# Kernel optimization log

Measured on AMD Instinct MI355X. Metric: run time of the kernel, lower is better.

## Reference

```python
import jax, jax.numpy as jnp
import numpy as np

B, T, D, H = 2048, 512, 32, 64


def _gru_layer(x, W_ih, W_hh, b_ih, b_hh):
    # x: [B, T, Din]; W_ih: [3H, Din]; W_hh: [3H, H]; gate order r, z, n (PyTorch).
    xp = jnp.einsum('btd,gd->btg', x, W_ih) + b_ih  # precompute input projections [B,T,3H]

    def step(h, xt):
        gh = h @ W_hh.T + b_hh                      # [B,3H]
        ir, iz, inn = jnp.split(xt, 3, axis=-1)
        hr, hz, hn = jnp.split(gh, 3, axis=-1)
        r = jax.nn.sigmoid(ir + hr)
        z = jax.nn.sigmoid(iz + hz)
        n = jnp.tanh(inn + r * hn)
        h_new = (1.0 - z) * n + z * h
        return h_new, h_new

    h0 = jnp.zeros((x.shape[0], W_hh.shape[1]), dtype=x.dtype)
    _, ys = jax.lax.scan(step, h0, xp.transpose(1, 0, 2))  # ys: [T,B,H]
    return ys.transpose(1, 0, 2)                           # [B,T,H]


def setup_inputs() -> dict:
    key = jax.random.key(0)
    ks = jax.random.split(key, 12)
    s_in = 1.0 / np.sqrt(H)
    u = lambda k, shp: jax.random.uniform(k, shp, jnp.float32, -s_in, s_in)
    return {
        'x': jax.random.normal(ks[0], (B, T, D), jnp.float32),
        'W_ih0': u(ks[1], (3 * H, D)),  'W_hh0': u(ks[2], (3 * H, H)),
        'b_ih0': u(ks[3], (3 * H,)),    'b_hh0': u(ks[4], (3 * H,)),
        'W_ih1': u(ks[5], (3 * H, H)),  'W_hh1': u(ks[6], (3 * H, H)),
        'b_ih1': u(ks[7], (3 * H,)),    'b_hh1': u(ks[8], (3 * H,)),
        'fc_w': u(ks[9], (1, H)),       'fc_b': u(ks[10], (1,)),
    }


def reference(x, W_ih0, W_hh0, b_ih0, b_hh0, W_ih1, W_hh1, b_ih1, b_hh1, fc_w, fc_b):
    # 2-layer GRU (eval mode: inter-layer dropout is identity) + linear head on last step.
    h1 = _gru_layer(x, W_ih0, W_hh0, b_ih0, b_hh0)   # [B,T,H]
    h2 = _gru_layer(h1, W_ih1, W_hh1, b_ih1, b_hh1)  # [B,T,H]
    out = h2[:, -1, :] @ fc_w.T + fc_b               # [B,1]
    return out[:, 0]                                  # [B]
```

## Files before the change

### kernel.cpp

```cpp
#include <hip/hip_runtime.h>

#define Bsz  2048
#define Tlen 512
#define Din  32
#define Hd   64
#define BT   16
#define HS   72
#define BUFE 2048
#define CHUNK 16
#define NCHUNK (Tlen / CHUNK)
#define XSTRH 1040
#define XBUFB (BT * XSTRH)

typedef _Float16 half8 __attribute__((ext_vector_type(8)));
typedef _Float16 half4 __attribute__((ext_vector_type(4)));
typedef float    f32x4 __attribute__((ext_vector_type(4)));

#define MFMA(a, b, c) __builtin_amdgcn_mfma_f32_16x16x32_f16((a), (b), (c), 0, 0, 0)

__device__ __forceinline__ half8 load8s(const float* p, float s) {
    half8 r;
#pragma unroll
    for (int j = 0; j < 8; ++j) r[j] = (_Float16)(p[j] * s);
    return r;
}
__device__ __forceinline__ half8 cvt8(float4 a, float4 b) {
    half8 r;
    r[0] = (_Float16)a.x; r[1] = (_Float16)a.y; r[2] = (_Float16)a.z; r[3] = (_Float16)a.w;
    r[4] = (_Float16)b.x; r[5] = (_Float16)b.y; r[6] = (_Float16)b.z; r[7] = (_Float16)b.w;
    return r;
}

__device__ __forceinline__ void gate_update(const f32x4& gr, const f32x4& gz,
                                            const f32x4& anx, const f32x4& anh,
                                            float hst[4], _Float16* dst, bool wr) {
    half4 pk;
#pragma unroll
    for (int r = 0; r < 4; ++r) {
        float Er = __builtin_amdgcn_exp2f(gr[r]);
        float rr = __builtin_amdgcn_rcpf(1.0f + Er);
        float yy = anx[r] + rr * anh[r];
        float En = __builtin_amdgcn_exp2f(yy);
        float Ez = __builtin_amdgcn_exp2f(gz[r]);
        float num = Ez * (1.0f - En) + hst[r] * (1.0f + En);
        float den = (1.0f + Ez) * (1.0f + En);
        hst[r] = num * __builtin_amdgcn_rcpf(den);
        pk[r] = (_Float16)hst[r];
    }
    if (wr) *(half4*)dst = pk;
}

__global__ __launch_bounds__(512, 2)
void gru_fused(const float* __restrict__ x,
               const float* __restrict__ Wih0, const float* __restrict__ Whh0,
               const float* __restrict__ bih0, const float* __restrict__ bhh0,
               const float* __restrict__ Wih1, const float* __restrict__ Whh1,
               const float* __restrict__ bih1, const float* __restrict__ bhh1,
               const float* __restrict__ fcw,  const float* __restrict__ fcb,
               float* __restrict__ out)
{
    __shared__ _Float16 arena[4 * BUFE];
    __shared__ __attribute__((aligned(16))) char xstage[2 * XBUFB];
    __shared__ float hfin[BT][Hd];

    const int tid  = threadIdx.x;
    const int lane = tid & 63;
    const int wave = tid >> 6;
    const int grp  = wave >> 2;
    const int wg   = wave & 3;
    const int m    = lane & 15;
    const int quad = lane >> 4;
    const int col  = (wg << 4) + m;
    const int gc   = (wg << 4) + (quad << 2);
    const int b0   = blockIdx.x << 4;

    for (int idx = tid; idx < 4 * BUFE; idx += 512) arena[idx] = (_Float16)0.f;

    const int sb    = (wave << 1) + (lane >> 5);
    const int st    = (lane & 31) >> 1;
    const int sdh   = lane & 1;
    const float* xgp = x + (size_t)(b0 + sb) * (Tlen * Din) + st * Din + sdh * 16;
    const int swoff = sb * XSTRH + st * 64 + sdh * 32;

    float4 xh0, xh1, xh2, xh3;
    {
        const float* p = xgp;
        xh0 = *(const float4*)p;       xh1 = *(const float4*)(p + 4);
        xh2 = *(const float4*)(p + 8); xh3 = *(const float4*)(p + 12);
        char* wp = xstage + swoff;
        *(half8*)wp        = cvt8(xh0, xh1);
        *(half8*)(wp + 16) = cvt8(xh2, xh3);
    }
    {
        const float* p = xgp + CHUNK * Din;
        xh0 = *(const float4*)p;       xh1 = *(const float4*)(p + 4);
        xh2 = *(const float4*)(p + 8); xh3 = *(const float4*)(p + 12);
        char* wp = xstage + XBUFB + swoff;
        *(half8*)wp        = cvt8(xh0, xh1);
        *(half8*)(wp + 16) = cvt8(xh2, xh3);
    }
    {
        const float* p = xgp + 2 * CHUNK * Din;
        xh0 = *(const float4*)p;       xh1 = *(const float4*)(p + 4);
        xh2 = *(const float4*)(p + 8); xh3 = *(const float4*)(p + 12);
    }

    const float sRZ = -1.44269504f;
    const float sN  = -2.88539008f;

    half8 wx[2][3], wh[2][3];
    f32x4 brz0v, brz1v, binv, bhnv;

    if (grp == 0) {
        wx[0][0] = load8s(Wih0 + (      col) * Din + quad * 8, sRZ);
        wx[0][1] = load8s(Wih0 + ( 64 + col) * Din + quad * 8, sRZ);
        wx[0][2] = load8s(Wih0 + (128 + col) * Din + quad * 8, sN);
#pragma unroll
        for (int kb = 0; kb < 2; ++kb) {
            wh[kb][0] = load8s(Whh0 + (      col) * Hd + kb * 32 + quad * 8, sRZ);
            wh[kb][1] = load8s(Whh0 + ( 64 + col) * Hd + kb * 32 + quad * 8, sRZ);
            wh[kb][2] = load8s(Whh0 + (128 + col) * Hd + kb * 32 + quad * 8, sN);
        }
#pragma unroll
        for (int r = 0; r < 4; ++r) {
            brz0v[r] = sRZ * (bih0[gc + r] + bhh0[gc + r]);
            brz1v[r] = sRZ * (bih0[64 + gc + r] + bhh0[64 + gc + r]);
            binv[r]  = sN * bih0[128 + gc + r];
            bhnv[r]  = sN * bhh0[128 + gc + r];
        }
    } else {
#pragma unroll
        for (int kb = 0; kb < 2; ++kb) {
            wx[kb][0] = load8s(Wih1 + (      col) * Hd + kb * 32 + quad * 8, sRZ);
            wx[kb][1] = load8s(Wih1 + ( 64 + col) * Hd + kb * 32 + quad * 8, sRZ);
            wx[kb][2] = load8s(Wih1 + (128 + col) * Hd + kb * 32 + quad * 8, sN);
            wh[kb][0] = load8s(Whh1 + (      col) * Hd + kb * 32 + quad * 8, sRZ);
            wh[kb][1] = load8s(Whh1 + ( 64 + col) * Hd + kb * 32 + quad * 8, sRZ);
            wh[kb][2] = load8s(Whh1 + (128 + col) * Hd + kb * 32 + quad * 8, sN);
        }
#pragma unroll
        for (int r = 0; r < 4; ++r) {
            brz0v[r] = sRZ * (bih1[gc + r] + bhh1[gc + r]);
            brz1v[r] = sRZ * (bih1[64 + gc + r] + bhh1[64 + gc + r]);
            binv[r]  = sN * bih1[128 + gc + r];
            bhnv[r]  = sN * bhh1[128 + gc + r];
        }
    }

    const int rdoff  = m * HS + quad * 8;
    const int xroffH = m * XSTRH + quad * 16;
    const int wroff  = m * HS + gc;
    float hst[4] = {0.f, 0.f, 0.f, 0.f};
    half8 ax;
    __syncthreads();

    if (grp == 0) ax = *(const half8*)(xstage + xroffH);

#define STEP(I, RO, WO)                                                          \
  do {                                                                           \
    if (grp == 0) {                                                              \
      const _Float16* s1 = arena + (RO) + rdoff;                                 \
      half8 bh0 = *(const half8*)s1;                                             \
      half8 bh1 = *(const half8*)(s1 + 32);                                      \
      f32x4 arx = brz0v, azx = brz1v, anx = binv;                                \
      f32x4 arh = {0.f,0.f,0.f,0.f}, azh = {0.f,0.f,0.f,0.f};                    \
      f32x4 anh = bhnv;                                                          \
      arh = MFMA(wh[0][0], bh0, arh); arh = MFMA(wh[1][0], bh1, arh);            \
      azh = MFMA(wh[0][1], bh0, azh); azh = MFMA(wh[1][1], bh1, azh);            \
      anh = MFMA(wh[0][2], bh0, anh); anh = MFMA(wh[1][2], bh1, anh);            \
      arx = MFMA(wx[0][0], ax, arx);                                             \
      azx = MFMA(wx[0][1], ax, azx);                                             \
      anx = MFMA(wx[0][2], ax, anx);                                             \
      f32x4 gr = arx + arh, gz = azx + azh;                                      \
      gate_update(gr, gz, anx, anh, hst, arena + (WO) + wroff, true);            \
      { const int nx = ((I) + 1 < Tlen) ? (I) + 1 : (I);                         \
        ax = *(const half8*)(xstage + ((nx >> 4) & 1) * XBUFB                    \
                             + (nx & 15) * 64 + xroffH); }                       \
    } else {                                                                     \
      const _Float16* s1 = arena + (RO) + rdoff;                    \
      const _Float16* s2 = s1 + 2 * BUFE;                           \
      half8 bx0 = *(const half8*)s1;                                             \
      half8 bx1 = *(const half8*)(s1 + 32);                                      \
      half8 bh0 = *(const half8*)s2;                                             \
      half8 bh1 = *(const half8*)(s2 + 32);                                      \
      f32x4 arx = brz0v, azx = brz1v, anx = binv;                                \
      f32x4 arh = {0.f,0.f,0.f,0.f}, azh = {0.f,0.f,0.f,0.f};                    \
      f32x4 anh = bhnv;                                                          \
      arx = MFMA(wx[0][0], bx0, arx); arx = MFMA(wx[1][0], bx1, arx);            \
      azx = MFMA(wx[0][1], bx0, azx); azx = MFMA(wx[1][1], bx1, azx);            \
      anx = MFMA(wx[0][2], bx0, anx); anx = MFMA(wx[1][2], bx1, anx);            \
      arh = MFMA(wh[0][0], bh0, arh); arh = MFMA(wh[1][0], bh1, arh);            \
      azh = MFMA(wh[0][1], bh0, azh); azh = MFMA(wh[1][1], bh1, azh);            \
      anh = MFMA(wh[0][2], bh0, anh); anh = MFMA(wh[1][2], bh1, anh);            \
      f32x4 gr = arx + arh, gz = azx + azh;                                      \
      gate_update(gr, gz, anx, anh, hst, arena + 2 * BUFE + (WO) + wroff,        \
                  true);                                                         \
    }                                                                            \
    __syncthreads();                                                             \
  } while (0)

    if (grp == 0) {
        f32x4 gr = brz0v, gz = brz1v, anx = binv, anh = bhnv;
        gr  = MFMA(wx[0][0], ax, gr);
        gz  = MFMA(wx[0][1], ax, gz);
        anx = MFMA(wx[0][2], ax, anx);
        gate_update(gr, gz, anx, anh, hst, arena + 0 + wroff, true);
        ax = *(const half8*)(xstage + 1 * 64 + xroffH);
    }
    __syncthreads();

    for (int i = 1; i + 1 < Tlen; i += 2) {
        STEP(i, 0, BUFE);
        if (((i + 1) & (CHUNK - 1)) == 0) {
            const int k = (i + 1) >> 4;
            if (k + 1 < NCHUNK) {
                char* wp = xstage + ((k + 1) & 1) * XBUFB + swoff;
                *(half8*)wp        = cvt8(xh0, xh1);
                *(half8*)(wp + 16) = cvt8(xh2, xh3);
            }
            if (k + 2 < NCHUNK) {
                const float* p = xgp + (size_t)(k + 2) * (CHUNK * Din);
                xh0 = *(const float4*)p;       xh1 = *(const float4*)(p + 4);
                xh2 = *(const float4*)(p + 8); xh3 = *(const float4*)(p + 12);
            }
        }
        STEP(i + 1, BUFE, 0);
    }
    STEP(Tlen - 1, 0, BUFE);

    if (grp == 1) {
        const _Float16* s1 = arena + BUFE + rdoff;
        const _Float16* s2 = s1 + 2 * BUFE;
        half8 bx0 = *(const half8*)s1;
        half8 bx1 = *(const half8*)(s1 + 32);
        half8 bh0 = *(const half8*)s2;
        half8 bh1 = *(const half8*)(s2 + 32);
        f32x4 arx = brz0v, azx = brz1v, anx = binv;
        f32x4 arh = {0.f,0.f,0.f,0.f}, azh = {0.f,0.f,0.f,0.f};
        f32x4 anh = bhnv;
        arx = MFMA(wx[0][0], bx0, arx); arx = MFMA(wx[1][0], bx1, arx);
        azx = MFMA(wx[0][1], bx0, azx); azx = MFMA(wx[1][1], bx1, azx);
        anx = MFMA(wx[0][2], bx0, anx); anx = MFMA(wx[1][2], bx1, anx);
        arh = MFMA(wh[0][0], bh0, arh); arh = MFMA(wh[1][0], bh1, arh);
        azh = MFMA(wh[0][1], bh0, azh); azh = MFMA(wh[1][1], bh1, azh);
        anh = MFMA(wh[0][2], bh0, anh); anh = MFMA(wh[1][2], bh1, anh);
        f32x4 gr = arx + arh, gz = azx + azh;
        gate_update(gr, gz, anx, anh, hst, nullptr, false);
        f32x4 fv;
#pragma unroll
        for (int r = 0; r < 4; ++r) fv[r] = hst[r];
        *(f32x4*)(&hfin[m][gc]) = fv;
    }
    __syncthreads();
    if (tid < BT) {
        float acc = fcb[0];
        for (int c = 0; c < Hd; ++c) acc += hfin[tid][c] * fcw[c];
        out[b0 + tid] = acc;
    }
#undef STEP
}

extern "C" void kernel_launch(void* const* d_in, const int* in_sizes, int n_in,
                              void* d_out, int out_size, void* d_ws, size_t ws_size,
                              hipStream_t stream) {
    gru_fused<<<dim3(Bsz / BT), dim3(512), 0, stream>>>(
        (const float*)d_in[0],
        (const float*)d_in[1], (const float*)d_in[2],
        (const float*)d_in[3], (const float*)d_in[4],
        (const float*)d_in[5], (const float*)d_in[6],
        (const float*)d_in[7], (const float*)d_in[8],
        (const float*)d_in[9], (const float*)d_in[10],
        (float*)d_out);
}
```

Before: 434.0 us.

## Process two 16-row batch tiles per block and load x directly per step

Each block now handles 32 batch rows as two interleaved 16-row tiles (A and B), so every wave issues two independent MFMA chains and gate updates per step. This is meant to hide MFMA and transcendental latency, and to halve the number of barriers per batch row. The chunked LDS staging of x is removed, and each lane instead prefetches its own x slice from global memory two steps ahead and converts it to half in registers. The grid shrinks to 64 blocks, leaving fewer blocks to spread across CUs. Register pressure also goes up, and the per-step global loads sit on the latency-critical path.

```diff
diff --git a/kernel.cpp b/kernel.cpp
--- a/kernel.cpp
+++ b/kernel.cpp
@@ -4,13 +4,9 @@
 #define Tlen 512
 #define Din  32
 #define Hd   64
-#define BT   16
+#define BT   32
 #define HS   72
 #define BUFE 2048
-#define CHUNK 16
-#define NCHUNK (Tlen / CHUNK)
-#define XSTRH 1040
-#define XBUFB (BT * XSTRH)
 
 typedef _Float16 half8 __attribute__((ext_vector_type(8)));
 typedef _Float16 half4 __attribute__((ext_vector_type(4)));
@@ -59,8 +55,7 @@
                const float* __restrict__ fcw,  const float* __restrict__ fcb,
                float* __restrict__ out)
 {
-    __shared__ _Float16 arena[4 * BUFE];
-    __shared__ __attribute__((aligned(16))) char xstage[2 * XBUFB];
+    __shared__ _Float16 arena[8 * BUFE];
     __shared__ float hfin[BT][Hd];
 
     const int tid  = threadIdx.x;
@@ -72,38 +67,9 @@
     const int quad = lane >> 4;
     const int col  = (wg << 4) + m;
     const int gc   = (wg << 4) + (quad << 2);
-    const int b0   = blockIdx.x << 4;
-
-    for (int idx = tid; idx < 4 * BUFE; idx += 512) arena[idx] = (_Float16)0.f;
-
-    const int sb    = (wave << 1) + (lane >> 5);
-    const int st    = (lane & 31) >> 1;
-    const int sdh   = lane & 1;
-    const float* xgp = x + (size_t)(b0 + sb) * (Tlen * Din) + st * Din + sdh * 16;
-    const int swoff = sb * XSTRH + st * 64 + sdh * 32;
-
-    float4 xh0, xh1, xh2, xh3;
-    {
-        const float* p = xgp;
-        xh0 = *(const float4*)p;       xh1 = *(const float4*)(p + 4);
-        xh2 = *(const float4*)(p + 8); xh3 = *(const float4*)(p + 12);
-        char* wp = xstage + swoff;
-        *(half8*)wp        = cvt8(xh0, xh1);
-        *(half8*)(wp + 16) = cvt8(xh2, xh3);
-    }
-    {
-        const float* p = xgp + CHUNK * Din;
-        xh0 = *(const float4*)p;       xh1 = *(const float4*)(p + 4);
-        xh2 = *(const float4*)(p + 8); xh3 = *(const float4*)(p + 12);
-        char* wp = xstage + XBUFB + swoff;
-        *(half8*)wp        = cvt8(xh0, xh1);
-        *(half8*)(wp + 16) = cvt8(xh2, xh3);
-    }
-    {
-        const float* p = xgp + 2 * CHUNK * Din;
-        xh0 = *(const float4*)p;       xh1 = *(const float4*)(p + 4);
-        xh2 = *(const float4*)(p + 8); xh3 = *(const float4*)(p + 12);
-    }
+    const int b0   = blockIdx.x << 5;
+
+    for (int idx = tid; idx < 8 * BUFE; idx += 512) arena[idx] = (_Float16)0.f;
 
     const float sRZ = -1.44269504f;
     const float sN  = -2.88539008f;
@@ -147,109 +113,149 @@
         }
     }
 
-    const int rdoff  = m * HS + quad * 8;
-    const int xroffH = m * XSTRH + quad * 16;
-    const int wroff  = m * HS + gc;
-    float hst[4] = {0.f, 0.f, 0.f, 0.f};
-    half8 ax;
+    const int rdoff = m * HS + quad * 8;
+    const int wroff = m * HS + gc;
+    float hstA[4] = {0.f, 0.f, 0.f, 0.f};
+    float hstB[4] = {0.f, 0.f, 0.f, 0.f};
+
+    const float* xgpA = x + (size_t)(b0 + m) * (Tlen * Din) + quad * 8;
+    const float* xgpB = xgpA + (size_t)16 * (Tlen * Din);
+    float4 xA0a, xA0b, xB0a, xB0b;
+    float4 xA1a, xA1b, xB1a, xB1b;
+    if (grp == 0) {
+        xA0a = *(const float4*)(xgpA);        xA0b = *(const float4*)(xgpA + 4);
+        xB0a = *(const float4*)(xgpB);        xB0b = *(const float4*)(xgpB + 4);
+        xA1a = *(const float4*)(xgpA + Din);  xA1b = *(const float4*)(xgpA + Din + 4);
+        xB1a = *(const float4*)(xgpB + Din);  xB1b = *(const float4*)(xgpB + Din + 4);
+    }
     __syncthreads();
 
-    if (grp == 0) ax = *(const half8*)(xstage + xroffH);
-
-#define STEP(I, RO, WO)                                                          \
+#define STEP(I, RO, WO, xAa, xAb, xBa, xBb)                                      \
   do {                                                                           \
     if (grp == 0) {                                                              \
-      const _Float16* s1 = arena + (RO) + rdoff;                                 \
-      half8 bh0 = *(const half8*)s1;                                             \
-      half8 bh1 = *(const half8*)(s1 + 32);                                      \
-      f32x4 arx = brz0v, azx = brz1v, anx = binv;                                \
-      f32x4 arh = {0.f,0.f,0.f,0.f}, azh = {0.f,0.f,0.f,0.f};                    \
-      f32x4 anh = bhnv;                                                          \
-      arh = MFMA(wh[0][0], bh0, arh); arh = MFMA(wh[1][0], bh1, arh);            \
-      azh = MFMA(wh[0][1], bh0, azh); azh = MFMA(wh[1][1], bh1, azh);            \
-      anh = MFMA(wh[0][2], bh0, anh); anh = MFMA(wh[1][2], bh1, anh);            \
-      arx = MFMA(wx[0][0], ax, arx);                                             \
-      azx = MFMA(wx[0][1], ax, azx);                                             \
-      anx = MFMA(wx[0][2], ax, anx);                                             \
-      f32x4 gr = arx + arh, gz = azx + azh;                                      \
-      gate_update(gr, gz, anx, anh, hst, arena + (WO) + wroff, true);            \
-      { const int nx = ((I) + 1 < Tlen) ? (I) + 1 : (I);                         \
-        ax = *(const half8*)(xstage + ((nx >> 4) & 1) * XBUFB                    \
-                             + (nx & 15) * 64 + xroffH); }                       \
+      const _Float16* sA = arena + (RO) + rdoff;                                 \
+      const _Float16* sB = sA + 4 * BUFE;                                        \
+      half8 bhA0 = *(const half8*)sA;                                            \
+      half8 bhA1 = *(const half8*)(sA + 32);                                     \
+      half8 bhB0 = *(const half8*)sB;                                            \
+      half8 bhB1 = *(const half8*)(sB + 32);                                     \
+      half8 axA = cvt8(xAa, xAb);                                                \
+      half8 axB = cvt8(xBa, xBb);                                                \
+      { const int nx = ((I) + 2 < Tlen) ? (I) + 2 : Tlen - 1;                    \
+        const float* pA = xgpA + (size_t)nx * Din;                               \
+        const float* pB = xgpB + (size_t)nx * Din;                               \
+        xAa = *(const float4*)pA; xAb = *(const float4*)(pA + 4);                \
+        xBa = *(const float4*)pB; xBb = *(const float4*)(pB + 4); }              \
+      f32x4 arhA = {0.f,0.f,0.f,0.f}, azhA = {0.f,0.f,0.f,0.f}, anhA = bhnv;     \
+      f32x4 arhB = {0.f,0.f,0.f,0.f}, azhB = {0.f,0.f,0.f,0.f}, anhB = bhnv;     \
+      arhA = MFMA(wh[0][0], bhA0, arhA); arhA = MFMA(wh[1][0], bhA1, arhA);      \
+      arhB = MFMA(wh[0][0], bhB0, arhB); arhB = MFMA(wh[1][0], bhB1, arhB);      \
+      azhA = MFMA(wh[0][1], bhA0, azhA); azhA = MFMA(wh[1][1], bhA1, azhA);      \
+      azhB = MFMA(wh[0][1], bhB0, azhB); azhB = MFMA(wh[1][1], bhB1, azhB);      \
+      anhA = MFMA(wh[0][2], bhA0, anhA); anhA = MFMA(wh[1][2], bhA1, anhA);      \
+      anhB = MFMA(wh[0][2], bhB0, anhB); anhB = MFMA(wh[1][2], bhB1, anhB);      \
+      f32x4 arxA = brz0v, azxA = brz1v, anxA = binv;                             \
+      f32x4 arxB = brz0v, azxB = brz1v, anxB = binv;                             \
+      arxA = MFMA(wx[0][0], axA, arxA);  arxB = MFMA(wx[0][0], axB, arxB);       \
+      azxA = MFMA(wx[0][1], axA, azxA);  azxB = MFMA(wx[0][1], axB, azxB);       \
+      anxA = MFMA(wx[0][2], axA, anxA);  anxB = MFMA(wx[0][2], axB, anxB);       \
+      f32x4 grA = arxA + arhA, gzA = azxA + azhA;                                \
+      f32x4 grB = arxB + arhB, gzB = azxB + azhB;                                \
+      gate_update(grA, gzA, anxA, anhA, hstA, arena + (WO) + wroff, true);       \
+      gate_update(grB, gzB, anxB, anhB, hstB,                                    \
+                  arena + 4 * BUFE + (WO) + wroff, true);                        \
     } else {                                                                     \
-      const _Float16* s1 = arena + (RO) + rdoff;                    \
-      const _Float16* s2 = s1 + 2 * BUFE;                           \
-      half8 bx0 = *(const half8*)s1;                                             \
-      half8 bx1 = *(const half8*)(s1 + 32);                                      \
-      half8 bh0 = *(const half8*)s2;                                             \
-      half8 bh1 = *(const half8*)(s2 + 32);                                      \
-      f32x4 arx = brz0v, azx = brz1v, anx = binv;                                \
-      f32x4 arh = {0.f,0.f,0.f,0.f}, azh = {0.f,0.f,0.f,0.f};                    \
-      f32x4 anh = bhnv;                                                          \
-      arx = MFMA(wx[0][0], bx0, arx); arx = MFMA(wx[1][0], bx1, arx);            \
-      azx = MFMA(wx[0][1], bx0, azx); azx = MFMA(wx[1][1], bx1, azx);            \
-      anx = MFMA(wx[0][2], bx0, anx); anx = MFMA(wx[1][2], bx1, anx);            \
-      arh = MFMA(wh[0][0], bh0, arh); arh = MFMA(wh[1][0], bh1, arh);            \
-      azh = MFMA(wh[0][1], bh0, azh); azh = MFMA(wh[1][1], bh1, azh);            \
-      anh = MFMA(wh[0][2], bh0, anh); anh = MFMA(wh[1][2], bh1, anh);            \
-      f32x4 gr = arx + arh, gz = azx + azh;                                      \
-      gate_update(gr, gz, anx, anh, hst, arena + 2 * BUFE + (WO) + wroff,        \
-                  true);                                                         \
+      const _Float16* s1A = arena + (RO) + rdoff;                  \
+      const _Float16* s2A = s1A + 2 * BUFE;                        \
+      const _Float16* s1B = s1A + 4 * BUFE;                                      \
+      const _Float16* s2B = s1B + 2 * BUFE;                                      \
+      half8 bxA0 = *(const half8*)s1A;                                           \
+      half8 bxA1 = *(const half8*)(s1A + 32);                                    \
+      half8 bhA0 = *(const half8*)s2A;                                           \
+      half8 bhA1 = *(const half8*)(s2A + 32);                                    \
+      half8 bxB0 = *(const half8*)s1B;                                           \
+      half8 bxB1 = *(const half8*)(s1B + 32);                                    \
+      half8 bhB0 = *(const half8*)s2B;                                           \
+      half8 bhB1 = *(const half8*)(s2B + 32);                                    \
+      f32x4 arxA = brz0v, azxA = brz1v, anxA = binv;                             \
+      f32x4 arhA = {0.f,0.f,0.f,0.f}, azhA = {0.f,0.f,0.f,0.f}, anhA = bhnv;     \
+      f32x4 arxB = brz0v, azxB = brz1v, anxB = binv;                             \
+      f32x4 arhB = {0.f,0.f,0.f,0.f}, azhB = {0.f,0.f,0.f,0.f}, anhB = bhnv;     \
+      arxA = MFMA(wx[0][0], bxA0, arxA); arxA = MFMA(wx[1][0], bxA1, arxA);      \
+      arxB = MFMA(wx[0][0], bxB0, arxB); arxB = MFMA(wx[1][0], bxB1, arxB);      \
+      azxA = MFMA(wx[0][1], bxA0, azxA); azxA = MFMA(wx[1][1], bxA1, azxA);      \
+      azxB = MFMA(wx[0][1], bxB0, azxB); azxB = MFMA(wx[1][1], bxB1, azxB);      \
+      anxA = MFMA(wx[0][2], bxA0, anxA); anxA = MFMA(wx[1][2], bxA1, anxA);      \
+      anxB = MFMA(wx[0][2], bxB0, anxB); anxB = MFMA(wx[1][2], bxB1, anxB);      \
+      arhA = MFMA(wh[0][0], bhA0, arhA); arhA = MFMA(wh[1][0], bhA1, arhA);      \
+      arhB = MFMA(wh[0][0], bhB0, arhB); arhB = MFMA(wh[1][0], bhB1, arhB);      \
+      azhA = MFMA(wh[0][1], bhA0, azhA); azhA = MFMA(wh[1][1], bhA1, azhA);      \
+      azhB = MFMA(wh[0][1], bhB0, azhB); azhB = MFMA(wh[1][1], bhB1, azhB);      \
+      anhA = MFMA(wh[0][2], bhA0, anhA); anhA = MFMA(wh[1][2], bhA1, anhA);      \
+      anhB = MFMA(wh[0][2], bhB0, anhB); anhB = MFMA(wh[1][2], bhB1, anhB);      \
+      f32x4 grA = arxA + arhA, gzA = azxA + azhA;                                \
+      f32x4 grB = arxB + arhB, gzB = azxB + azhB;                                \
+      gate_update(grA, gzA, anxA, anhA, hstA,                                    \
+                  arena + 2 * BUFE + (WO) + wroff, true);                        \
+      gate_update(grB, gzB, anxB, anhB, hstB,                                    \
+                  arena + 6 * BUFE + (WO) + wroff, true);                        \
     }                                                                            \
     __syncthreads();                                                             \
   } while (0)
 
     if (grp == 0) {
-        f32x4 gr = brz0v, gz = brz1v, anx = binv, anh = bhnv;
-        gr  = MFMA(wx[0][0], ax, gr);
-        gz  = MFMA(wx[0][1], ax, gz);
-        anx = MFMA(wx[0][2], ax, anx);
-        gate_update(gr, gz, anx, anh, hst, arena + 0 + wroff, true);
-        ax = *(const half8*)(xstage + 1 * 64 + xroffH);
+        half8 axA = cvt8(xA0a, xA0b);
+        half8 axB = cvt8(xB0a, xB0b);
+        {
+            const float* pA = xgpA + 2 * Din;
+            const float* pB = xgpB + 2 * Din;
+            xA0a = *(const float4*)pA; xA0b = *(const float4*)(pA + 4);
+            xB0a = *(const float4*)pB; xB0b = *(const float4*)(pB + 4);
+        }
+        f32x4 grA = brz0v, gzA = brz1v, anxA = binv, anhA = bhnv;
+        grA  = MFMA(wx[0][0], axA, grA);
+        gzA  = MFMA(wx[0][1], axA, gzA);
+        anxA = MFMA(wx[0][2], axA, anxA);
+        gate_update(grA, gzA, anxA, anhA, hstA, arena + 0 + wroff, true);
+        f32x4 grB = brz0v, gzB = brz1v, anxB = binv, anhB = bhnv;
+        grB  = MFMA(wx[0][0], axB, grB);
+        gzB  = MFMA(wx[0][1], axB, gzB);
+        anxB = MFMA(wx[0][2], axB, anxB);
+        gate_update(grB, gzB, anxB, anhB, hstB, arena + 4 * BUFE + wroff, true);
     }
     __syncthreads();
 
     for (int i = 1; i + 1 < Tlen; i += 2) {
-        STEP(i, 0, BUFE);
-        if (((i + 1) & (CHUNK - 1)) == 0) {
-            const int k = (i + 1) >> 4;
-            if (k + 1 < NCHUNK) {
-                char* wp = xstage + ((k + 1) & 1) * XBUFB + swoff;
-                *(half8*)wp        = cvt8(xh0, xh1);
-                *(half8*)(wp + 16) = cvt8(xh2, xh3);
-            }
-            if (k + 2 < NCHUNK) {
-                const float* p = xgp + (size_t)(k + 2) * (CHUNK * Din);
-                xh0 = *(const float4*)p;       xh1 = *(const float4*)(p + 4);
-                xh2 = *(const float4*)(p + 8); xh3 = *(const float4*)(p + 12);
-            }
-        }
-        STEP(i + 1, BUFE, 0);
-    }
-    STEP(Tlen - 1, 0, BUFE);
+        STEP(i,     0,    BUFE, xA1a, xA1b, xB1a, xB1b);
+        STEP(i + 1, BUFE, 0,    xA0a, xA0b, xB0a, xB0b);
+    }
+    STEP(Tlen - 1, 0, BUFE, xA1a, xA1b, xB1a, xB1b);
 
     if (grp == 1) {
-        const _Float16* s1 = arena + BUFE + rdoff;
-        const _Float16* s2 = s1 + 2 * BUFE;
-        half8 bx0 = *(const half8*)s1;
-        half8 bx1 = *(const half8*)(s1 + 32);
-        half8 bh0 = *(const half8*)s2;
-        half8 bh1 = *(const half8*)(s2 + 32);
-        f32x4 arx = brz0v, azx = brz1v, anx = binv;
-        f32x4 arh = {0.f,0.f,0.f,0.f}, azh = {0.f,0.f,0.f,0.f};
-        f32x4 anh = bhnv;
-        arx = MFMA(wx[0][0], bx0, arx); arx = MFMA(wx[1][0], bx1, arx);
-        azx = MFMA(wx[0][1], bx0, azx); azx = MFMA(wx[1][1], bx1, azx);
-        anx = MFMA(wx[0][2], bx0, anx); anx = MFMA(wx[1][2], bx1, anx);
-        arh = MFMA(wh[0][0], bh0, arh); arh = MFMA(wh[1][0], bh1, arh);
-        azh = MFMA(wh[0][1], bh0, azh); azh = MFMA(wh[1][1], bh1, azh);
-        anh = MFMA(wh[0][2], bh0, anh); anh = MFMA(wh[1][2], bh1, anh);
-        f32x4 gr = arx + arh, gz = azx + azh;
-        gate_update(gr, gz, anx, anh, hst, nullptr, false);
-        f32x4 fv;
-#pragma unroll
-        for (int r = 0; r < 4; ++r) fv[r] = hst[r];
-        *(f32x4*)(&hfin[m][gc]) = fv;
+#pragma unroll
+        for (int t = 0; t < 2; ++t) {
+            const _Float16* s1 = arena + t * 4 * BUFE + BUFE + rdoff;
+            const _Float16* s2 = s1 + 2 * BUFE;
+            half8 bx0 = *(const half8*)s1;
+            half8 bx1 = *(const half8*)(s1 + 32);
+            half8 bh0 = *(const half8*)s2;
+            half8 bh1 = *(const half8*)(s2 + 32);
+            f32x4 arx = brz0v, azx = brz1v, anx = binv;
+            f32x4 arh = {0.f,0.f,0.f,0.f}, azh = {0.f,0.f,0.f,0.f}, anh = bhnv;
+            arx = MFMA(wx[0][0], bx0, arx); arx = MFMA(wx[1][0], bx1, arx);
+            azx = MFMA(wx[0][1], bx0, azx); azx = MFMA(wx[1][1], bx1, azx);
+            anx = MFMA(wx[0][2], bx0, anx); anx = MFMA(wx[1][2], bx1, anx);
+            arh = MFMA(wh[0][0], bh0, arh); arh = MFMA(wh[1][0], bh1, arh);
+            azh = MFMA(wh[0][1], bh0, azh); azh = MFMA(wh[1][1], bh1, azh);
+            anh = MFMA(wh[0][2], bh0, anh); anh = MFMA(wh[1][2], bh1, anh);
+            f32x4 gr = arx + arh, gz = azx + azh;
+            float* hs = t ? hstB : hstA;
+            gate_update(gr, gz, anx, anh, hs, nullptr, false);
+            f32x4 fv;
+#pragma unroll
+            for (int r = 0; r < 4; ++r) fv[r] = hs[r];
+            *(f32x4*)(&hfin[t * 16 + m][gc]) = fv;
+        }
     }
     __syncthreads();
     if (tid < BT) {
```

Measured after the change: 640.8 us. 1.48x slower.

## Replace block barriers with LDS atomic counters between GRU layer wave groups

Applied to the files above, without the earlier changes.

Drops the per-step __syncthreads that locked layer-0 and layer-1 wave groups in step. Each side now spins on workgroup-scope LDS counters, so layer 0 can run up to a few steps ahead of layer 1 through a 4-slot h1 ring. The LDS staging of x is also removed: layer-0 waves load their x row directly from global memory two steps ahead and convert it in registers. This adds spin-wait overhead and atomics, and the bounded spin count could silently break ordering if a wait ever exceeds it.

```diff
diff --git a/kernel.cpp b/kernel.cpp
--- a/kernel.cpp
+++ b/kernel.cpp
@@ -6,11 +6,8 @@
 #define Hd   64
 #define BT   16
 #define HS   72
-#define BUFE 2048
-#define CHUNK 16
-#define NCHUNK (Tlen / CHUNK)
-#define XSTRH 1040
-#define XBUFB (BT * XSTRH)
+#define SLOT (BT * HS)
+#define SPINB (1 << 14)
 
 typedef _Float16 half8 __attribute__((ext_vector_type(8)));
 typedef _Float16 half4 __attribute__((ext_vector_type(4)));
@@ -31,9 +28,9 @@
     return r;
 }
 
-__device__ __forceinline__ void gate_update(const f32x4& gr, const f32x4& gz,
-                                            const f32x4& anx, const f32x4& anh,
-                                            float hst[4], _Float16* dst, bool wr) {
+__device__ __forceinline__ half4 gate_upd(const f32x4& gr, const f32x4& gz,
+                                          const f32x4& anx, const f32x4& anh,
+                                          float hst[4]) {
     half4 pk;
 #pragma unroll
     for (int r = 0; r < 4; ++r) {
@@ -47,8 +44,24 @@
         hst[r] = num * __builtin_amdgcn_rcpf(den);
         pk[r] = (_Float16)hst[r];
     }
-    if (wr) *(half4*)dst = pk;
-}
+    return pk;
+}
+
+#define SPIN_GE(CTR, TGT, CACHE)                                         \
+  do {                                                                   \
+    if ((CACHE) < (TGT)) {                                               \
+      int v_ = (CACHE);                                                  \
+      for (int sp_ = 0; v_ < (TGT) && sp_ < SPINB; ++sp_) {              \
+        if (lane == 0)                                                   \
+          v_ = __hip_atomic_load(&CTR, __ATOMIC_ACQUIRE,                 \
+                                 __HIP_MEMORY_SCOPE_WORKGROUP);          \
+        v_ = __builtin_amdgcn_readfirstlane(v_);                         \
+        if (v_ < (TGT)) __builtin_amdgcn_s_sleep(1);                     \
+      }                                                                  \
+      (CACHE) = v_;                                                      \
+    }                                                                    \
+    __builtin_amdgcn_sched_barrier(0);                                   \
+  } while (0)
 
 __global__ __launch_bounds__(512, 2)
 void gru_fused(const float* __restrict__ x,
@@ -59,9 +72,10 @@
                const float* __restrict__ fcw,  const float* __restrict__ fcb,
                float* __restrict__ out)
 {
-    __shared__ _Float16 arena[4 * BUFE];
-    __shared__ __attribute__((aligned(16))) char xstage[2 * XBUFB];
+    __shared__ _Float16 h1r[4 * SLOT];
+    __shared__ _Float16 h2r[2 * SLOT];
     __shared__ float hfin[BT][Hd];
+    __shared__ int c1, c2, u1;
 
     const int tid  = threadIdx.x;
     const int lane = tid & 63;
@@ -74,47 +88,26 @@
     const int gc   = (wg << 4) + (quad << 2);
     const int b0   = blockIdx.x << 4;
 
-    for (int idx = tid; idx < 4 * BUFE; idx += 512) arena[idx] = (_Float16)0.f;
-
-    const int sb    = (wave << 1) + (lane >> 5);
-    const int st    = (lane & 31) >> 1;
-    const int sdh   = lane & 1;
-    const float* xgp = x + (size_t)(b0 + sb) * (Tlen * Din) + st * Din + sdh * 16;
-    const int swoff = sb * XSTRH + st * 64 + sdh * 32;
-
-    float4 xh0, xh1, xh2, xh3;
-    {
-        const float* p = xgp;
-        xh0 = *(const float4*)p;       xh1 = *(const float4*)(p + 4);
-        xh2 = *(const float4*)(p + 8); xh3 = *(const float4*)(p + 12);
-        char* wp = xstage + swoff;
-        *(half8*)wp        = cvt8(xh0, xh1);
-        *(half8*)(wp + 16) = cvt8(xh2, xh3);
+    for (int idx = tid; idx < SLOT; idx += 512) {
+        h1r[3 * SLOT + idx] = (_Float16)0.f;
+        h2r[SLOT + idx]     = (_Float16)0.f;
     }
-    {
-        const float* p = xgp + CHUNK * Din;
-        xh0 = *(const float4*)p;       xh1 = *(const float4*)(p + 4);
-        xh2 = *(const float4*)(p + 8); xh3 = *(const float4*)(p + 12);
-        char* wp = xstage + XBUFB + swoff;
-        *(half8*)wp        = cvt8(xh0, xh1);
-        *(half8*)(wp + 16) = cvt8(xh2, xh3);
-    }
-    {
-        const float* p = xgp + 2 * CHUNK * Din;
-        xh0 = *(const float4*)p;       xh1 = *(const float4*)(p + 4);
-        xh2 = *(const float4*)(p + 8); xh3 = *(const float4*)(p + 12);
-    }
+    if (tid == 0) { c1 = 0; c2 = 0; u1 = 0; }
 
     const float sRZ = -1.44269504f;
     const float sN  = -2.88539008f;
-
-    half8 wx[2][3], wh[2][3];
-    f32x4 brz0v, brz1v, binv, bhnv;
+    const int rdoff = m * HS + quad * 8;
+    const int wroff = m * HS + gc;
+    float hst[4] = {0.f, 0.f, 0.f, 0.f};
+
+    __syncthreads();
 
     if (grp == 0) {
-        wx[0][0] = load8s(Wih0 + (      col) * Din + quad * 8, sRZ);
-        wx[0][1] = load8s(Wih0 + ( 64 + col) * Din + quad * 8, sRZ);
-        wx[0][2] = load8s(Wih0 + (128 + col) * Din + quad * 8, sN);
+        half8 wx0, wx1, wx2, wh[2][3];
+        f32x4 brz0v, brz1v, binv, bhnv;
+        wx0 = load8s(Wih0 + (      col) * Din + quad * 8, sRZ);
+        wx1 = load8s(Wih0 + ( 64 + col) * Din + quad * 8, sRZ);
+        wx2 = load8s(Wih0 + (128 + col) * Din + quad * 8, sN);
 #pragma unroll
         for (int kb = 0; kb < 2; ++kb) {
             wh[kb][0] = load8s(Whh0 + (      col) * Hd + kb * 32 + quad * 8, sRZ);
@@ -128,7 +121,48 @@
             binv[r]  = sN * bih0[128 + gc + r];
             bhnv[r]  = sN * bhh0[128 + gc + r];
         }
+        const float* xgp = x + (size_t)(b0 + m) * (Tlen * Din) + quad * 8;
+        float4 x0a, x0b, x1a, x1b;
+        x0a = *(const float4*)(xgp);        x0b = *(const float4*)(xgp + 4);
+        x1a = *(const float4*)(xgp + Din);  x1b = *(const float4*)(xgp + Din + 4);
+        int c1v = 0, u1v = 0;
+
+#define STEP_A(T, xa_, xb_)                                              \
+  do {                                                                   \
+    SPIN_GE(c1, 4 * (T), c1v);                \
+    const _Float16* s1 = h1r + (((T) + 3) & 3) * SLOT + rdoff;           \
+    half8 bh0 = *(const half8*)s1;                                       \
+    half8 bh1 = *(const half8*)(s1 + 32);                                \
+    half8 ax = cvt8(xa_, xb_);                                           \
+    { const int nx = ((T) + 2 < Tlen) ? (T) + 2 : Tlen - 1;              \
+      const float* p = xgp + (size_t)nx * Din;                           \
+      xa_ = *(const float4*)p; xb_ = *(const float4*)(p + 4); }          \
+    f32x4 arx = brz0v, azx = brz1v, anx = binv;                          \
+    f32x4 arh = {0.f,0.f,0.f,0.f}, azh = {0.f,0.f,0.f,0.f}, anh = bhnv;  \
+    arh = MFMA(wh[0][0], bh0, arh); arh = MFMA(wh[1][0], bh1, arh);      \
+    azh = MFMA(wh[0][1], bh0, azh); azh = MFMA(wh[1][1], bh1, azh);      \
+    anh = MFMA(wh[0][2], bh0, anh); anh = MFMA(wh[1][2], bh1, anh);      \
+    arx = MFMA(wx0, ax, arx);                                            \
+    azx = MFMA(wx1, ax, azx);                                            \
+    anx = MFMA(wx2, ax, anx);                                            \
+    f32x4 gr = arx + arh, gz = azx + azh;                                \
+    half4 pk = gate_upd(gr, gz, anx, anh, hst);                          \
+    SPIN_GE(u1, 4 * ((T) - 3), u1v);          \
+    *(half4*)(h1r + ((T) & 3) * SLOT + wroff) = pk;                      \
+    asm volatile("s_waitcnt lgkmcnt(0)" ::: "memory");                   \
+    if (lane == 0)                                                       \
+      __hip_atomic_fetch_add(&c1, 1, __ATOMIC_RELEASE,                   \
+                             __HIP_MEMORY_SCOPE_WORKGROUP);              \
+  } while (0)
+
+        for (int t = 0; t < Tlen; t += 2) {
+            STEP_A(t,     x0a, x0b);
+            STEP_A(t + 1, x1a, x1b);
+        }
+#undef STEP_A
     } else {
+        half8 wx[2][3], wh[2][3];
+        f32x4 brz0v, brz1v, binv, bhnv;
 #pragma unroll
         for (int kb = 0; kb < 2; ++kb) {
             wx[kb][0] = load8s(Wih1 + (      col) * Hd + kb * 32 + quad * 8, sRZ);
@@ -145,119 +179,59 @@
             binv[r]  = sN * bih1[128 + gc + r];
             bhnv[r]  = sN * bhh1[128 + gc + r];
         }
+        int c1v = 0, c2v = 0;
+
+#define STEP_B(T)                                                        \
+  do {                                                                   \
+    SPIN_GE(c2, 4 * (T), c2v);                \
+    SPIN_GE(c1, 4 * ((T) + 1), c1v);          \
+    const _Float16* s1 = h1r + ((T) & 3) * SLOT + rdoff;    \
+    const _Float16* s2 = h2r + (((T) + 1) & 1) * SLOT + rdoff;  \
+    half8 bx0 = *(const half8*)s1;                                       \
+    half8 bx1 = *(const half8*)(s1 + 32);                                \
+    half8 bh0 = *(const half8*)s2;                                       \
+    half8 bh1 = *(const half8*)(s2 + 32);                                \
+    f32x4 arx = brz0v, azx = brz1v, anx = binv;                          \
+    f32x4 arh = {0.f,0.f,0.f,0.f}, azh = {0.f,0.f,0.f,0.f}, anh = bhnv;  \
+    arx = MFMA(wx[0][0], bx0, arx); arx = MFMA(wx[1][0], bx1, arx);      \
+    azx = MFMA(wx[0][1], bx0, azx); azx = MFMA(wx[1][1], bx1, azx);      \
+    anx = MFMA(wx[0][2], bx0, anx); anx = MFMA(wx[1][2], bx1, anx);      \
+    arh = MFMA(wh[0][0], bh0, arh); arh = MFMA(wh[1][0], bh1, arh);      \
+    azh = MFMA(wh[0][1], bh0, azh); azh = MFMA(wh[1][1], bh1, azh);      \
+    anh = MFMA(wh[0][2], bh0, anh); anh = MFMA(wh[1][2], bh1, anh);      \
+    asm volatile("s_waitcnt lgkmcnt(0)" ::: "memory");   \
+    if (lane == 0)                                                       \
+      __hip_atomic_fetch_add(&u1, 1, __ATOMIC_RELEASE,                   \
+                             __HIP_MEMORY_SCOPE_WORKGROUP);              \
+    f32x4 gr = arx + arh, gz = azx + azh;                                \
+    half4 pk = gate_upd(gr, gz, anx, anh, hst);                          \
+    *(half4*)(h2r + ((T) & 1) * SLOT + wroff) = pk;                      \
+    if ((T) == Tlen - 1) {                                               \
+      f32x4 fv;                                                          \
+      for (int r = 0; r < 4; ++r) fv[r] = hst[r];                        \
+      *(f32x4*)(&hfin[m][gc]) = fv;                                      \
+    }                                                                    \
+    asm volatile("s_waitcnt lgkmcnt(0)" ::: "memory");                   \
+    if (lane == 0)                                                       \
+      __hip_atomic_fetch_add(&c2, 1, __ATOMIC_RELEASE,                   \
+                             __HIP_MEMORY_SCOPE_WORKGROUP);              \
+  } while (0)
+
+        for (int t = 0; t < Tlen; t += 2) {
+            STEP_B(t);
+            STEP_B(t + 1);
+        }
+#undef STEP_B
+
+        if (wg == 0) {
+            SPIN_GE(c2, 4 * Tlen, c2v);
+            if (lane < BT) {
+                float acc = fcb[0];
+                for (int c = 0; c < Hd; ++c) acc += hfin[lane][c] * fcw[c];
+                out[b0 + lane] = acc;
+            }
+        }
     }
-
-    const int rdoff  = m * HS + quad * 8;
-    const int xroffH = m * XSTRH + quad * 16;
-    const int wroff  = m * HS + gc;
-    float hst[4] = {0.f, 0.f, 0.f, 0.f};
-    half8 ax;
-    __syncthreads();
-
-    if (grp == 0) ax = *(const half8*)(xstage + xroffH);
-
-#define STEP(I, RO, WO)                                                          \
-  do {                                                                           \
-    if (grp == 0) {                                                              \
-      const _Float16* s1 = arena + (RO) + rdoff;                                 \
-      half8 bh0 = *(const half8*)s1;                                             \
-      half8 bh1 = *(const half8*)(s1 + 32);                                      \
-      f32x4 arx = brz0v, azx = brz1v, anx = binv;                                \
-      f32x4 arh = {0.f,0.f,0.f,0.f}, azh = {0.f,0.f,0.f,0.f};                    \
-      f32x4 anh = bhnv;                                                          \
-      arh = MFMA(wh[0][0], bh0, arh); arh = MFMA(wh[1][0], bh1, arh);            \
-      azh = MFMA(wh[0][1], bh0, azh); azh = MFMA(wh[1][1], bh1, azh);            \
-      anh = MFMA(wh[0][2], bh0, anh); anh = MFMA(wh[1][2], bh1, anh);            \
-      arx = MFMA(wx[0][0], ax, arx);                                             \
-      azx = MFMA(wx[0][1], ax, azx);                                             \
-      anx = MFMA(wx[0][2], ax, anx);                                             \
-      f32x4 gr = arx + arh, gz = azx + azh;                                      \
-      gate_update(gr, gz, anx, anh, hst, arena + (WO) + wroff, true);            \
-      { const int nx = ((I) + 1 < Tlen) ? (I) + 1 : (I);                         \
-        ax = *(const half8*)(xstage + ((nx >> 4) & 1) * XBUFB                    \
-                             + (nx & 15) * 64 + xroffH); }                       \
-    } else {                                                                     \
-      const _Float16* s1 = arena + (RO) + rdoff;                    \
-      const _Float16* s2 = s1 + 2 * BUFE;                           \
-      half8 bx0 = *(const half8*)s1;                                             \
-      half8 bx1 = *(const half8*)(s1 + 32);                                      \
-      half8 bh0 = *(const half8*)s2;                                             \
-      half8 bh1 = *(const half8*)(s2 + 32);                                      \
-      f32x4 arx = brz0v, azx = brz1v, anx = binv;                                \
-      f32x4 arh = {0.f,0.f,0.f,0.f}, azh = {0.f,0.f,0.f,0.f};                    \
-      f32x4 anh = bhnv;                                                          \
-      arx = MFMA(wx[0][0], bx0, arx); arx = MFMA(wx[1][0], bx1, arx);            \
-      azx = MFMA(wx[0][1], bx0, azx); azx = MFMA(wx[1][1], bx1, azx);            \
-      anx = MFMA(wx[0][2], bx0, anx); anx = MFMA(wx[1][2], bx1, anx);            \
-      arh = MFMA(wh[0][0], bh0, arh); arh = MFMA(wh[1][0], bh1, arh);            \
-      azh = MFMA(wh[0][1], bh0, azh); azh = MFMA(wh[1][1], bh1, azh);            \
-      anh = MFMA(wh[0][2], bh0, anh); anh = MFMA(wh[1][2], bh1, anh);            \
-      f32x4 gr = arx + arh, gz = azx + azh;                                      \
-      gate_update(gr, gz, anx, anh, hst, arena + 2 * BUFE + (WO) + wroff,        \
-                  true);                                                         \
-    }                                                                            \
-    __syncthreads();                                                             \
-  } while (0)
-
-    if (grp == 0) {
-        f32x4 gr = brz0v, gz = brz1v, anx = binv, anh = bhnv;
-        gr  = MFMA(wx[0][0], ax, gr);
-        gz  = MFMA(wx[0][1], ax, gz);
-        anx = MFMA(wx[0][2], ax, anx);
-        gate_update(gr, gz, anx, anh, hst, arena + 0 + wroff, true);
-        ax = *(const half8*)(xstage + 1 * 64 + xroffH);
-    }
-    __syncthreads();
-
-    for (int i = 1; i + 1 < Tlen; i += 2) {
-        STEP(i, 0, BUFE);
-        if (((i + 1) & (CHUNK - 1)) == 0) {
-            const int k = (i + 1) >> 4;
-            if (k + 1 < NCHUNK) {
-                char* wp = xstage + ((k + 1) & 1) * XBUFB + swoff;
-                *(half8*)wp        = cvt8(xh0, xh1);
-                *(half8*)(wp + 16) = cvt8(xh2, xh3);
-            }
-            if (k + 2 < NCHUNK) {
-                const float* p = xgp + (size_t)(k + 2) * (CHUNK * Din);
-                xh0 = *(const float4*)p;       xh1 = *(const float4*)(p + 4);
-                xh2 = *(const float4*)(p + 8); xh3 = *(const float4*)(p + 12);
-            }
-        }
-        STEP(i + 1, BUFE, 0);
-    }
-    STEP(Tlen - 1, 0, BUFE);
-
-    if (grp == 1) {
-        const _Float16* s1 = arena + BUFE + rdoff;
-        const _Float16* s2 = s1 + 2 * BUFE;
-        half8 bx0 = *(const half8*)s1;
-        half8 bx1 = *(const half8*)(s1 + 32);
-        half8 bh0 = *(const half8*)s2;
-        half8 bh1 = *(const half8*)(s2 + 32);
-        f32x4 arx = brz0v, azx = brz1v, anx = binv;
-        f32x4 arh = {0.f,0.f,0.f,0.f}, azh = {0.f,0.f,0.f,0.f};
-        f32x4 anh = bhnv;
-        arx = MFMA(wx[0][0], bx0, arx); arx = MFMA(wx[1][0], bx1, arx);
-        azx = MFMA(wx[0][1], bx0, azx); azx = MFMA(wx[1][1], bx1, azx);
-        anx = MFMA(wx[0][2], bx0, anx); anx = MFMA(wx[1][2], bx1, anx);
-        arh = MFMA(wh[0][0], bh0, arh); arh = MFMA(wh[1][0], bh1, arh);
-        azh = MFMA(wh[0][1], bh0, azh); azh = MFMA(wh[1][1], bh1, azh);
-        anh = MFMA(wh[0][2], bh0, anh); anh = MFMA(wh[1][2], bh1, anh);
-        f32x4 gr = arx + arh, gz = azx + azh;
-        gate_update(gr, gz, anx, anh, hst, nullptr, false);
-        f32x4 fv;
-#pragma unroll
-        for (int r = 0; r < 4; ++r) fv[r] = hst[r];
-        *(f32x4*)(&hfin[m][gc]) = fv;
-    }
-    __syncthreads();
-    if (tid < BT) {
-        float acc = fcb[0];
-        for (int c = 0; c < Hd; ++c) acc += hfin[tid][c] * fcw[c];
-        out[b0 + tid] = acc;
-    }
-#undef STEP
 }
 
 extern "C" void kernel_launch(void* const* d_in, const int* in_sizes, int n_in,
```

After: 535.8 us. +23.4%, slower.
